# Kernel optimization log

Hardware: AMD Instinct MI355X
Metric: run time of the kernel (lower is better)

Reference implementation:

```python
import jax, jax.numpy as jnp
import numpy as np

NUM_CLASSES = 80
BBOX_W, OBJ_W, CLS_W = 2.0, 1.0, 0.5
ALPHA, GAMMA = 0.25, 2.0


def setup_inputs() -> dict:
    key = jax.random.key(0)
    ks = jax.random.split(key, 8)
    B, T = 32, 64
    return {
        "cls_p4": jax.random.normal(ks[0], (B, 1 + NUM_CLASSES, 80, 80), jnp.float32),
        "reg_p4": jax.random.normal(ks[1], (B, 4, 80, 80), jnp.float32),
        "cls_p5": jax.random.normal(ks[2], (B, 1 + NUM_CLASSES, 40, 40), jnp.float32),
        "reg_p5": jax.random.normal(ks[3], (B, 4, 40, 40), jnp.float32),
        "t4_cls": jax.random.randint(ks[4], (B, T), 0, NUM_CLASSES, jnp.int32),
        "t4_box": jax.random.uniform(ks[5], (B, T, 4), jnp.float32),
        "t4_mask": jnp.ones((B, T), jnp.float32),
        "t5_cls": jax.random.randint(ks[6], (B, T), 0, NUM_CLASSES, jnp.int32),
        "t5_box": jax.random.uniform(ks[7], (B, T, 4), jnp.float32),
        "t5_mask": jnp.ones((B, T), jnp.float32),
    }


def _bce_logits(x, t):
    # stable BCEWithLogits: log(1+e^x) - x*t
    return jnp.logaddexp(0.0, x) - x * t


def _scale_loss(cls_p, reg_p, cls_ids, box, mask):
    B, C, H, W = cls_p.shape
    tx = box[..., 0] * W  # [B,T]
    ty = box[..., 1] * H
    tw = box[..., 2] * W
    th = box[..., 3] * H
    gx = jnp.clip(tx, 0, W - 1).astype(jnp.int32)
    gy = jnp.clip(ty, 0, H - 1).astype(jnp.int32)
    bb = jnp.arange(B)[:, None]  # [B,1] broadcast over T

    # gather per-target reg/cls vectors: [B,T,4] and [B,T,C]
    rv = jnp.transpose(reg_p, (0, 2, 3, 1))[bb, gy, gx]
    cv = jnp.transpose(cls_p, (0, 2, 3, 1))[bb, gy, gx]

    dx = jax.nn.sigmoid(rv[..., 0])
    dy = jax.nn.sigmoid(rv[..., 1])
    dw = jnp.exp(jnp.clip(rv[..., 2], -4.0, 4.0))
    dh = jnp.exp(jnp.clip(rv[..., 3], -4.0, 4.0))
    px = gx.astype(jnp.float32) + dx
    py = gy.astype(jnp.float32) + dy
    pred_box = jnp.stack([px - dw / 2, py - dh / 2, px + dw / 2, py + dh / 2], -1)
    tgt_box = jnp.stack([tx - tw / 2, ty - th / 2, tx + tw / 2, ty + th / 2], -1)

    d = pred_box - tgt_box
    sl1 = jnp.where(jnp.abs(d) < 1.0, 0.5 * d * d, jnp.abs(d) - 0.5).mean(-1)  # [B,T]
    lb = (sl1 * mask).sum()

    # objectness loss at target cells (target = 1)
    obj_t = cv[..., 0]
    lo = (jax.nn.softplus(-obj_t) * mask).sum()

    # focal classification loss
    onehot = jax.nn.one_hot(cls_ids, C - 1, dtype=cls_p.dtype)  # [B,T,NC]
    logits = cv[..., 1:]
    bce = _bce_logits(logits, onehot)
    p = jax.nn.sigmoid(logits)
    pt = p * onehot + (1.0 - p) * (1.0 - onehot)
    focal = (ALPHA * (1.0 - pt) ** GAMMA * bce).mean(-1)  # [B,T]
    lc = (focal * mask).sum()

    n = mask.sum()

    # background objectness: cells not hit by any valid target
    obj_map = jnp.zeros((B, H, W), cls_p.dtype).at[bb, gy, gx].max(mask)
    bg = obj_map == 0
    bg_cnt = bg.sum()
    bce_bg = jnp.where(bg, jax.nn.softplus(cls_p[:, 0]), 0.0).sum()
    lo = lo + 0.05 * jnp.where(bg_cnt > 0, bce_bg / jnp.maximum(bg_cnt, 1), 0.0)
    return lb, lo, lc, n


def reference(cls_p4, reg_p4, cls_p5, reg_p5,
              t4_cls, t4_box, t4_mask, t5_cls, t5_box, t5_mask):
    lb4, lo4, lc4, n4 = _scale_loss(cls_p4, reg_p4, t4_cls, t4_box, t4_mask)
    lb5, lo5, lc5, n5 = _scale_loss(cls_p5, reg_p5, t5_cls, t5_box, t5_mask)
    lb, lo, lc, n = lb4 + lb5, lo4 + lo5, lc4 + lc5, n4 + n5
    lb = jnp.where(n > 0, lb / jnp.maximum(n, 1), lb)
    lc = jnp.where(n > 0, lc / jnp.maximum(n, 1), lc)
    lo = lo / jnp.maximum(n, 1.0)
    total = BBOX_W * lb + OBJ_W * lo + CLS_W * lc
    return total
```

## Files before the change

### kernel.cpp

```cpp
#include <hip/hip_runtime.h>
#include <math.h>

#define NUM_CLASSES 80
#define C_CH (NUM_CLASSES + 1)

__device__ __forceinline__ float softplusf(float x) {
    return fmaxf(x, 0.f) + log1pf(expf(-fabsf(x)));
}
__device__ __forceinline__ float sigmoidf_(float x) {
    return 1.f / (1.f + expf(-x));
}


__global__ void fused_kernel(
    const float* __restrict__ cls_p4, const float* __restrict__ reg_p4,
    const float* __restrict__ cls_p5, const float* __restrict__ reg_p5,
    const int* __restrict__ t4_cls, const float* __restrict__ t4_box, const float* __restrict__ t4_mask,
    const int* __restrict__ t5_cls, const float* __restrict__ t5_box, const float* __restrict__ t5_mask,
    float* __restrict__ bgpart, float* __restrict__ tpart,
    int B, int T, int nbg4, int nbg5)
{
    const int tid = threadIdx.x;
    const int nbg = nbg4 + nbg5;

    if ((int)blockIdx.x < nbg) {
        const int blk = blockIdx.x;
        float sp = 0.f;
        if (blk < nbg4) {
            int b = blk / 25, j = blk - b * 25;
            int cell = j * 256 + tid;
            sp = softplusf(cls_p4[(size_t)b * (C_CH * 6400) + cell]);
        } else {
            int o = blk - nbg4;
            int b = o / 7, j = o - b * 7;
            int cell = j * 256 + tid;
            if (cell < 1600)
                sp = softplusf(cls_p5[(size_t)b * (C_CH * 1600) + cell]);
        }
        for (int off = 32; off > 0; off >>= 1) sp += __shfl_down(sp, off, 64);
        __shared__ float ss[4];
        if ((tid & 63) == 0) ss[tid >> 6] = sp;
        __syncthreads();
        if (tid == 0) bgpart[blockIdx.x] = ss[0] + ss[1] + ss[2] + ss[3];
        return;
    }

    const int BT = B * T;
    const int wave = tid >> 6;
    const int lane = tid & 63;
    const int tg = ((int)blockIdx.x - nbg) * 4 + wave;

    float lb = 0.f, lo = 0.f, lcv = 0.f, msum = 0.f;

    if (tg < 2 * BT) {
        const int scale = (tg >= BT) ? 1 : 0;
        const int ti = scale ? tg - BT : tg;
        const int b = ti / T;

        const float* cls_p; const float* reg_p; const int* tc; const float* tb_; const float* tm;
        int H, W;
        if (!scale) { cls_p = cls_p4; reg_p = reg_p4; tc = t4_cls; tb_ = t4_box; tm = t4_mask; H = 80; W = 80; }
        else        { cls_p = cls_p5; reg_p = reg_p5; tc = t5_cls; tb_ = t5_box; tm = t5_mask; H = 40; W = 40; }
        const int HW = H * W;

        const float mask = tm[ti];
        const int   cid  = tc[ti];
        const float bx0 = tb_[ti * 4 + 0], bx1 = tb_[ti * 4 + 1];
        const float bx2 = tb_[ti * 4 + 2], bx3 = tb_[ti * 4 + 3];

        const float tx = bx0 * (float)W, ty = bx1 * (float)H;
        const float tw = bx2 * (float)W, th = bx3 * (float)H;
        const int gx = (int)fminf(fmaxf(tx, 0.f), (float)(W - 1));
        const int gy = (int)fminf(fmaxf(ty, 0.f), (float)(H - 1));
        const int cell = gy * W + gx;

        const float* cvbase = cls_p + (size_t)b * C_CH * HW + cell;

        float rvq = 0.f;
        if (lane < 4) rvq = reg_p[(size_t)(b * 4 + lane) * HW + cell];
        float objq = (lane == 0) ? cvbase[0] : 0.f;

        float fsum = 0.f;
        for (int c = lane; c < NUM_CLASSES; c += 64) {
            float x   = cvbase[(size_t)(c + 1) * HW];
            float tgt = (c == cid) ? 1.f : 0.f;
            float bce = softplusf(x) - x * tgt;
            float p   = sigmoidf_(x);
            float pt  = p * tgt + (1.f - p) * (1.f - tgt);
            float om  = 1.f - pt;
            fsum += 0.25f * om * om * bce;
        }
        for (int off = 32; off > 0; off >>= 1) fsum += __shfl_down(fsum, off, 64);

        float rv0 = __shfl(rvq, 0, 64), rv1 = __shfl(rvq, 1, 64);
        float rv2 = __shfl(rvq, 2, 64), rv3 = __shfl(rvq, 3, 64);

        if (lane == 0) {
            lcv = (fsum * (1.f / (float)NUM_CLASSES)) * mask;
            lo  = softplusf(-objq) * mask;

            float dx = sigmoidf_(rv0), dy = sigmoidf_(rv1);
            float dw = expf(fminf(fmaxf(rv2, -4.f), 4.f));
            float dh = expf(fminf(fmaxf(rv3, -4.f), 4.f));
            float px = (float)gx + dx, py = (float)gy + dy;
            float pb0 = px - dw * 0.5f, pb1 = py - dh * 0.5f, pb2 = px + dw * 0.5f, pb3 = py + dh * 0.5f;
            float tb0 = tx - tw * 0.5f, tb1 = ty - th * 0.5f, tb2 = tx + tw * 0.5f, tb3 = ty + th * 0.5f;
            float s = 0.f, d, a;
            d = pb0 - tb0; a = fabsf(d); s += (a < 1.f) ? 0.5f * d * d : a - 0.5f;
            d = pb1 - tb1; a = fabsf(d); s += (a < 1.f) ? 0.5f * d * d : a - 0.5f;
            d = pb2 - tb2; a = fabsf(d); s += (a < 1.f) ? 0.5f * d * d : a - 0.5f;
            d = pb3 - tb3; a = fabsf(d); s += (a < 1.f) ? 0.5f * d * d : a - 0.5f;
            lb = (s * 0.25f) * mask;
            msum = mask;
        }
    }

    __shared__ float s4[4][4];
    if (lane == 0) { s4[wave][0] = lb; s4[wave][1] = lo; s4[wave][2] = lcv; s4[wave][3] = msum; }
    __syncthreads();
    if (tid < 4) {
        float v = s4[0][tid] + s4[1][tid] + s4[2][tid] + s4[3][tid];
        tpart[((int)blockIdx.x - nbg) * 4 + tid] = v;
    }
}

#define HASH_SZ 8192

__global__ void __launch_bounds__(1024) final_kernel(
    const float* __restrict__ cls_p4, const float* __restrict__ cls_p5,
    const float* __restrict__ t4_box, const float* __restrict__ t4_mask,
    const float* __restrict__ t5_box, const float* __restrict__ t5_mask,
    const float* __restrict__ bgpart, int nbg4, int nbg5,
    const float* __restrict__ tpart, int nT4,
    int B, int T, float* __restrict__ out)
{
    __shared__ unsigned int hash[HASH_SZ];
    __shared__ float red[16][12];
    const int tid = threadIdx.x;
    const int BT = B * T;

    for (int i = tid; i < HASH_SZ; i += 1024) hash[i] = 0u;
    __syncthreads();

    float occ_sp4 = 0.f, occ_c4 = 0.f, occ_sp5 = 0.f, occ_c5 = 0.f;
    for (int g = tid; g < 2 * BT; g += 1024) {
        const int scale = (g >= BT) ? 1 : 0;
        const int ti = scale ? g - BT : g;
        const float* tb_ = scale ? t5_box : t4_box;
        const float* tm  = scale ? t5_mask : t4_mask;
        const float mask = tm[ti];
        if (mask > 0.f) {
            const int b = ti / T;
            const int W = scale ? 40 : 80, H = W;
            const int HW = W * H;
            const float tx = tb_[ti * 4 + 0] * (float)W;
            const float ty = tb_[ti * 4 + 1] * (float)H;
            const int gx = (int)fminf(fmaxf(tx, 0.f), (float)(W - 1));
            const int gy = (int)fminf(fmaxf(ty, 0.f), (float)(H - 1));
            const int cell = gy * W + gx;
            const unsigned int id = ((unsigned)scale << 18) | (unsigned)(b * HW + cell);
            const unsigned int key = id + 1u;
            unsigned int h = (id * 2654435761u) >> 19;
            h &= (HASH_SZ - 1);
            for (;;) {
                unsigned int old = atomicCAS(&hash[h], 0u, key);
                if (old == 0u) {
                    const float* cls_p = scale ? cls_p5 : cls_p4;
                    float sp = softplusf(cls_p[(size_t)b * C_CH * HW + cell]);
                    if (scale) { occ_sp5 += sp; occ_c5 += 1.f; }
                    else       { occ_sp4 += sp; occ_c4 += 1.f; }
                    break;
                }
                if (old == key) break;
                h = (h + 1) & (HASH_SZ - 1);
            }
        }
    }

    float lb = 0.f, lo = 0.f, lc = 0.f, n = 0.f, bg4 = 0.f, bg5 = 0.f;
    for (int i = tid; i < nT4; i += 1024) {
        lb += tpart[i * 4 + 0]; lo += tpart[i * 4 + 1];
        lc += tpart[i * 4 + 2]; n  += tpart[i * 4 + 3];
    }
    for (int i = tid; i < nbg4; i += 1024) bg4 += bgpart[i];
    for (int i = tid; i < nbg5; i += 1024) bg5 += bgpart[nbg4 + i];

    float vals[10] = { lb, lo, lc, n, bg4, bg5, occ_sp4, occ_c4, occ_sp5, occ_c5 };
    #pragma unroll
    for (int k = 0; k < 10; k++) {
        float v = vals[k];
        for (int off = 32; off > 0; off >>= 1) v += __shfl_down(v, off, 64);
        vals[k] = v;
    }
    if ((tid & 63) == 0) {
        #pragma unroll
        for (int k = 0; k < 10; k++) red[tid >> 6][k] = vals[k];
    }
    __syncthreads();
    if (tid == 0) {
        float t[10];
        #pragma unroll
        for (int k = 0; k < 10; k++) {
            float s = 0.f;
            for (int w = 0; w < 16; w++) s += red[w][k];
            t[k] = s;
        }
        float lbt = t[0], lot = t[1], lct = t[2], nt = t[3];
        float bce_bg4 = t[4] - t[6];
        float bce_bg5 = t[5] - t[8];
        float cnt4 = (float)(B * 6400) - t[7];
        float cnt5 = (float)(B * 1600) - t[9];
        lot += 0.05f * ((cnt4 > 0.f) ? bce_bg4 / fmaxf(cnt4, 1.f) : 0.f);
        lot += 0.05f * ((cnt5 > 0.f) ? bce_bg5 / fmaxf(cnt5, 1.f) : 0.f);
        float nd = fmaxf(nt, 1.f);
        if (nt > 0.f) { lbt /= nd; lct /= nd; }
        lot /= fmaxf(nt, 1.f);
        out[0] = 2.0f * lbt + 1.0f * lot + 0.5f * lct;
    }
}

extern "C" void kernel_launch(void* const* d_in, const int* in_sizes, int n_in,
                              void* d_out, int out_size, void* d_ws, size_t ws_size,
                              hipStream_t stream) {
    const float* cls_p4 = (const float*)d_in[0];
    const float* reg_p4 = (const float*)d_in[1];
    const float* cls_p5 = (const float*)d_in[2];
    const float* reg_p5 = (const float*)d_in[3];
    const int*   t4_cls = (const int*)d_in[4];
    const float* t4_box = (const float*)d_in[5];
    const float* t4_mask= (const float*)d_in[6];
    const int*   t5_cls = (const int*)d_in[7];
    const float* t5_box = (const float*)d_in[8];
    const float* t5_mask= (const float*)d_in[9];

    const int B = in_sizes[0] / (C_CH * 6400);
    const int T = in_sizes[4] / B;
    const int BT = B * T;

    const int nbg4 = B * 25;
    const int nbg5 = B * 7;
    const int nTblk = (2 * BT + 3) / 4;

    float* bgpart = (float*)d_ws;
    float* tpart  = bgpart + (nbg4 + nbg5);

    fused_kernel<<<nbg4 + nbg5 + nTblk, 256, 0, stream>>>(
        cls_p4, reg_p4, cls_p5, reg_p5,
        t4_cls, t4_box, t4_mask, t5_cls, t5_box, t5_mask,
        bgpart, tpart, B, T, nbg4, nbg5);

    final_kernel<<<1, 1024, 0, stream>>>(
        cls_p4, cls_p5, t4_box, t4_mask, t5_box, t5_mask,
        bgpart, nbg4, nbg5, tpart, nTblk, B, T, (float*)d_out);
}
```

Baseline: 148.0 us.

## Move occupied-cell dedup from single-block hash into parallel per-batch waves

Background-cell deduplication moves out of the single-block final kernel's shared-memory atomic hash table. Extra blocks in the main kernel now handle it, one wave per (scale, batch) pair, using a quadratic first-occurrence scan over the targets. The final kernel shrinks to a 256-thread reduction of partial sums. Targets per batch are capped at MAX_T; above that cap the occupied-cell correction is silently skipped.

```diff
diff --git a/kernel.cpp b/kernel.cpp
--- a/kernel.cpp
+++ b/kernel.cpp
@@ -3,6 +3,7 @@
 
 #define NUM_CLASSES 80
 #define C_CH (NUM_CLASSES + 1)
+#define MAX_T 128
 
 __device__ __forceinline__ float softplusf(float x) {
     return fmaxf(x, 0.f) + log1pf(expf(-fabsf(x)));
@@ -17,11 +18,14 @@
     const float* __restrict__ cls_p5, const float* __restrict__ reg_p5,
     const int* __restrict__ t4_cls, const float* __restrict__ t4_box, const float* __restrict__ t4_mask,
     const int* __restrict__ t5_cls, const float* __restrict__ t5_box, const float* __restrict__ t5_mask,
-    float* __restrict__ bgpart, float* __restrict__ tpart,
-    int B, int T, int nbg4, int nbg5)
+    float* __restrict__ bgpart, float* __restrict__ tpart, float* __restrict__ occpart,
+    int B, int T, int nbg4, int nbg5, int nTblk)
 {
-    const int tid = threadIdx.x;
-    const int nbg = nbg4 + nbg5;
+    const int tid  = threadIdx.x;
+    const int wave = tid >> 6;
+    const int lane = tid & 63;
+    const int nbg  = nbg4 + nbg5;
+    const int BT   = B * T;
 
     if ((int)blockIdx.x < nbg) {
         const int blk = blockIdx.x;
@@ -39,153 +43,165 @@
         }
         for (int off = 32; off > 0; off >>= 1) sp += __shfl_down(sp, off, 64);
         __shared__ float ss[4];
-        if ((tid & 63) == 0) ss[tid >> 6] = sp;
+        if (lane == 0) ss[wave] = sp;
         __syncthreads();
         if (tid == 0) bgpart[blockIdx.x] = ss[0] + ss[1] + ss[2] + ss[3];
         return;
     }
 
-    const int BT = B * T;
-    const int wave = tid >> 6;
-    const int lane = tid & 63;
-    const int tg = ((int)blockIdx.x - nbg) * 4 + wave;
-
-    float lb = 0.f, lo = 0.f, lcv = 0.f, msum = 0.f;
-
-    if (tg < 2 * BT) {
-        const int scale = (tg >= BT) ? 1 : 0;
-        const int ti = scale ? tg - BT : tg;
-        const int b = ti / T;
-
-        const float* cls_p; const float* reg_p; const int* tc; const float* tb_; const float* tm;
-        int H, W;
-        if (!scale) { cls_p = cls_p4; reg_p = reg_p4; tc = t4_cls; tb_ = t4_box; tm = t4_mask; H = 80; W = 80; }
-        else        { cls_p = cls_p5; reg_p = reg_p5; tc = t5_cls; tb_ = t5_box; tm = t5_mask; H = 40; W = 40; }
-        const int HW = H * W;
-
-        const float mask = tm[ti];
-        const int   cid  = tc[ti];
-        const float bx0 = tb_[ti * 4 + 0], bx1 = tb_[ti * 4 + 1];
-        const float bx2 = tb_[ti * 4 + 2], bx3 = tb_[ti * 4 + 3];
-
-        const float tx = bx0 * (float)W, ty = bx1 * (float)H;
-        const float tw = bx2 * (float)W, th = bx3 * (float)H;
-        const int gx = (int)fminf(fmaxf(tx, 0.f), (float)(W - 1));
-        const int gy = (int)fminf(fmaxf(ty, 0.f), (float)(H - 1));
-        const int cell = gy * W + gx;
-
-        const float* cvbase = cls_p + (size_t)b * C_CH * HW + cell;
-
-        float rvq = 0.f;
-        if (lane < 4) rvq = reg_p[(size_t)(b * 4 + lane) * HW + cell];
-        float objq = (lane == 0) ? cvbase[0] : 0.f;
-
-        float fsum = 0.f;
-        for (int c = lane; c < NUM_CLASSES; c += 64) {
-            float x   = cvbase[(size_t)(c + 1) * HW];
-            float tgt = (c == cid) ? 1.f : 0.f;
-            float bce = softplusf(x) - x * tgt;
-            float p   = sigmoidf_(x);
-            float pt  = p * tgt + (1.f - p) * (1.f - tgt);
-            float om  = 1.f - pt;
-            fsum += 0.25f * om * om * bce;
-        }
-        for (int off = 32; off > 0; off >>= 1) fsum += __shfl_down(fsum, off, 64);
-
-        float rv0 = __shfl(rvq, 0, 64), rv1 = __shfl(rvq, 1, 64);
-        float rv2 = __shfl(rvq, 2, 64), rv3 = __shfl(rvq, 3, 64);
-
-        if (lane == 0) {
-            lcv = (fsum * (1.f / (float)NUM_CLASSES)) * mask;
-            lo  = softplusf(-objq) * mask;
-
-            float dx = sigmoidf_(rv0), dy = sigmoidf_(rv1);
-            float dw = expf(fminf(fmaxf(rv2, -4.f), 4.f));
-            float dh = expf(fminf(fmaxf(rv3, -4.f), 4.f));
-            float px = (float)gx + dx, py = (float)gy + dy;
-            float pb0 = px - dw * 0.5f, pb1 = py - dh * 0.5f, pb2 = px + dw * 0.5f, pb3 = py + dh * 0.5f;
-            float tb0 = tx - tw * 0.5f, tb1 = ty - th * 0.5f, tb2 = tx + tw * 0.5f, tb3 = ty + th * 0.5f;
-            float s = 0.f, d, a;
-            d = pb0 - tb0; a = fabsf(d); s += (a < 1.f) ? 0.5f * d * d : a - 0.5f;
-            d = pb1 - tb1; a = fabsf(d); s += (a < 1.f) ? 0.5f * d * d : a - 0.5f;
-            d = pb2 - tb2; a = fabsf(d); s += (a < 1.f) ? 0.5f * d * d : a - 0.5f;
-            d = pb3 - tb3; a = fabsf(d); s += (a < 1.f) ? 0.5f * d * d : a - 0.5f;
-            lb = (s * 0.25f) * mask;
-            msum = mask;
-        }
-    }
-
-    __shared__ float s4[4][4];
-    if (lane == 0) { s4[wave][0] = lb; s4[wave][1] = lo; s4[wave][2] = lcv; s4[wave][3] = msum; }
-    __syncthreads();
-    if (tid < 4) {
-        float v = s4[0][tid] + s4[1][tid] + s4[2][tid] + s4[3][tid];
-        tpart[((int)blockIdx.x - nbg) * 4 + tid] = v;
-    }
-}
-
-#define HASH_SZ 8192
-
-__global__ void __launch_bounds__(1024) final_kernel(
-    const float* __restrict__ cls_p4, const float* __restrict__ cls_p5,
-    const float* __restrict__ t4_box, const float* __restrict__ t4_mask,
-    const float* __restrict__ t5_box, const float* __restrict__ t5_mask,
-    const float* __restrict__ bgpart, int nbg4, int nbg5,
-    const float* __restrict__ tpart, int nT4,
-    int B, int T, float* __restrict__ out)
-{
-    __shared__ unsigned int hash[HASH_SZ];
-    __shared__ float red[16][12];
-    const int tid = threadIdx.x;
-    const int BT = B * T;
-
-    for (int i = tid; i < HASH_SZ; i += 1024) hash[i] = 0u;
-    __syncthreads();
-
-    float occ_sp4 = 0.f, occ_c4 = 0.f, occ_sp5 = 0.f, occ_c5 = 0.f;
-    for (int g = tid; g < 2 * BT; g += 1024) {
-        const int scale = (g >= BT) ? 1 : 0;
-        const int ti = scale ? g - BT : g;
-        const float* tb_ = scale ? t5_box : t4_box;
-        const float* tm  = scale ? t5_mask : t4_mask;
-        const float mask = tm[ti];
-        if (mask > 0.f) {
+    if ((int)blockIdx.x < nbg + nTblk) {
+        const int tg = ((int)blockIdx.x - nbg) * 4 + wave;
+        float lb = 0.f, lo = 0.f, lcv = 0.f, msum = 0.f;
+
+        if (tg < 2 * BT) {
+            const int scale = (tg >= BT) ? 1 : 0;
+            const int ti = scale ? tg - BT : tg;
             const int b = ti / T;
-            const int W = scale ? 40 : 80, H = W;
-            const int HW = W * H;
-            const float tx = tb_[ti * 4 + 0] * (float)W;
-            const float ty = tb_[ti * 4 + 1] * (float)H;
+
+            const float* cls_p; const float* reg_p; const int* tc; const float* tb_; const float* tm;
+            int H, W;
+            if (!scale) { cls_p = cls_p4; reg_p = reg_p4; tc = t4_cls; tb_ = t4_box; tm = t4_mask; H = 80; W = 80; }
+            else        { cls_p = cls_p5; reg_p = reg_p5; tc = t5_cls; tb_ = t5_box; tm = t5_mask; H = 40; W = 40; }
+            const int HW = H * W;
+
+            const float mask = tm[ti];
+            const int   cid  = tc[ti];
+            const float bx0 = tb_[ti * 4 + 0], bx1 = tb_[ti * 4 + 1];
+            const float bx2 = tb_[ti * 4 + 2], bx3 = tb_[ti * 4 + 3];
+
+            const float tx = bx0 * (float)W, ty = bx1 * (float)H;
+            const float tw = bx2 * (float)W, th = bx3 * (float)H;
             const int gx = (int)fminf(fmaxf(tx, 0.f), (float)(W - 1));
             const int gy = (int)fminf(fmaxf(ty, 0.f), (float)(H - 1));
             const int cell = gy * W + gx;
-            const unsigned int id = ((unsigned)scale << 18) | (unsigned)(b * HW + cell);
-            const unsigned int key = id + 1u;
-            unsigned int h = (id * 2654435761u) >> 19;
-            h &= (HASH_SZ - 1);
-            for (;;) {
-                unsigned int old = atomicCAS(&hash[h], 0u, key);
-                if (old == 0u) {
-                    const float* cls_p = scale ? cls_p5 : cls_p4;
-                    float sp = softplusf(cls_p[(size_t)b * C_CH * HW + cell]);
-                    if (scale) { occ_sp5 += sp; occ_c5 += 1.f; }
-                    else       { occ_sp4 += sp; occ_c4 += 1.f; }
-                    break;
+
+            const float* cvbase = cls_p + (size_t)b * C_CH * HW + cell;
+
+            float rvq = 0.f;
+            if (lane < 4) rvq = reg_p[(size_t)(b * 4 + lane) * HW + cell];
+            float objq = (lane == 0) ? cvbase[0] : 0.f;
+
+            float fsum = 0.f;
+            for (int c = lane; c < NUM_CLASSES; c += 64) {
+                float x   = cvbase[(size_t)(c + 1) * HW];
+                float tgt = (c == cid) ? 1.f : 0.f;
+                float bce = softplusf(x) - x * tgt;
+                float p   = sigmoidf_(x);
+                float pt  = p * tgt + (1.f - p) * (1.f - tgt);
+                float om  = 1.f - pt;
+                fsum += 0.25f * om * om * bce;
+            }
+            for (int off = 32; off > 0; off >>= 1) fsum += __shfl_down(fsum, off, 64);
+
+            float rv0 = __shfl(rvq, 0, 64), rv1 = __shfl(rvq, 1, 64);
+            float rv2 = __shfl(rvq, 2, 64), rv3 = __shfl(rvq, 3, 64);
+
+            if (lane == 0) {
+                lcv = (fsum * (1.f / (float)NUM_CLASSES)) * mask;
+                lo  = softplusf(-objq) * mask;
+
+                float dx = sigmoidf_(rv0), dy = sigmoidf_(rv1);
+                float dw = expf(fminf(fmaxf(rv2, -4.f), 4.f));
+                float dh = expf(fminf(fmaxf(rv3, -4.f), 4.f));
+                float px = (float)gx + dx, py = (float)gy + dy;
+                float pb0 = px - dw * 0.5f, pb1 = py - dh * 0.5f, pb2 = px + dw * 0.5f, pb3 = py + dh * 0.5f;
+                float tb0 = tx - tw * 0.5f, tb1 = ty - th * 0.5f, tb2 = tx + tw * 0.5f, tb3 = ty + th * 0.5f;
+                float s = 0.f, d, a;
+                d = pb0 - tb0; a = fabsf(d); s += (a < 1.f) ? 0.5f * d * d : a - 0.5f;
+                d = pb1 - tb1; a = fabsf(d); s += (a < 1.f) ? 0.5f * d * d : a - 0.5f;
+                d = pb2 - tb2; a = fabsf(d); s += (a < 1.f) ? 0.5f * d * d : a - 0.5f;
+                d = pb3 - tb3; a = fabsf(d); s += (a < 1.f) ? 0.5f * d * d : a - 0.5f;
+                lb = (s * 0.25f) * mask;
+                msum = mask;
+            }
+        }
+
+        __shared__ float s4[4][4];
+        if (lane == 0) { s4[wave][0] = lb; s4[wave][1] = lo; s4[wave][2] = lcv; s4[wave][3] = msum; }
+        __syncthreads();
+        if (tid < 4) {
+            float v = s4[0][tid] + s4[1][tid] + s4[2][tid] + s4[3][tid];
+            tpart[((int)blockIdx.x - nbg) * 4 + tid] = v;
+        }
+        return;
+    }
+
+    {
+        __shared__ unsigned int cells[4][MAX_T];
+        const int p = ((int)blockIdx.x - nbg - nTblk) * 4 + wave;
+        float osp = 0.f, ocnt = 0.f;
+        bool valid_pair = (p < 2 * B) && (T <= MAX_T);
+        int scale = 0, b = 0;
+        const float* tb_ = nullptr; const float* tm = nullptr;
+        int W = 80, HW = 6400;
+        if (valid_pair) {
+            scale = p / B; b = p - scale * B;
+            tb_ = scale ? t5_box : t4_box;
+            tm  = scale ? t5_mask : t4_mask;
+            W = scale ? 40 : 80; HW = W * W;
+            for (int i = lane; i < T; i += 64) {
+                const int ti = b * T + i;
+                unsigned int cellv = 0xFFFFFFFFu;
+                if (tm[ti] > 0.f) {
+                    const float tx = tb_[ti * 4 + 0] * (float)W;
+                    const float ty = tb_[ti * 4 + 1] * (float)W;
+                    const int gx = (int)fminf(fmaxf(tx, 0.f), (float)(W - 1));
+                    const int gy = (int)fminf(fmaxf(ty, 0.f), (float)(W - 1));
+                    cellv = (unsigned)(gy * W + gx);
                 }
-                if (old == key) break;
-                h = (h + 1) & (HASH_SZ - 1);
-            }
-        }
-    }
-
-    float lb = 0.f, lo = 0.f, lc = 0.f, n = 0.f, bg4 = 0.f, bg5 = 0.f;
-    for (int i = tid; i < nT4; i += 1024) {
+                cells[wave][i] = cellv;
+            }
+        }
+        __syncthreads();
+        if (valid_pair) {
+            const float* cls_p = scale ? cls_p5 : cls_p4;
+            for (int i = lane; i < T; i += 64) {
+                unsigned int cv = cells[wave][i];
+                if (cv != 0xFFFFFFFFu) {
+                    bool first = true;
+                    for (int j = 0; j < i; j++)
+                        if (cells[wave][j] == cv) { first = false; break; }
+                    if (first) {
+                        osp  += softplusf(cls_p[(size_t)b * C_CH * HW + (int)cv]);
+                        ocnt += 1.f;
+                    }
+                }
+            }
+        }
+        for (int off = 32; off > 0; off >>= 1) {
+            osp  += __shfl_down(osp,  off, 64);
+            ocnt += __shfl_down(ocnt, off, 64);
+        }
+        if (lane == 0 && p < 2 * B) {
+            occpart[p * 2]     = osp;
+            occpart[p * 2 + 1] = ocnt;
+        }
+    }
+}
+
+__global__ void __launch_bounds__(256) final_kernel(
+    const float* __restrict__ bgpart, int nbg4, int nbg5,
+    const float* __restrict__ tpart, int nTblk,
+    const float* __restrict__ occpart,
+    int B, float* __restrict__ out)
+{
+    const int tid = threadIdx.x;
+    float lb = 0.f, lo = 0.f, lc = 0.f, n = 0.f;
+    float bg4 = 0.f, bg5 = 0.f, o4 = 0.f, c4 = 0.f, o5 = 0.f, c5 = 0.f;
+
+    for (int i = tid; i < nTblk; i += 256) {
         lb += tpart[i * 4 + 0]; lo += tpart[i * 4 + 1];
         lc += tpart[i * 4 + 2]; n  += tpart[i * 4 + 3];
     }
-    for (int i = tid; i < nbg4; i += 1024) bg4 += bgpart[i];
-    for (int i = tid; i < nbg5; i += 1024) bg5 += bgpart[nbg4 + i];
-
-    float vals[10] = { lb, lo, lc, n, bg4, bg5, occ_sp4, occ_c4, occ_sp5, occ_c5 };
+    for (int i = tid; i < nbg4; i += 256) bg4 += bgpart[i];
+    for (int i = tid; i < nbg5; i += 256) bg5 += bgpart[nbg4 + i];
+    for (int p = tid; p < 2 * B; p += 256) {
+        if (p < B) { o4 += occpart[p * 2]; c4 += occpart[p * 2 + 1]; }
+        else       { o5 += occpart[p * 2]; c5 += occpart[p * 2 + 1]; }
+    }
+
+    __shared__ float red[4][10];
+    float vals[10] = { lb, lo, lc, n, bg4, bg5, o4, c4, o5, c5 };
     #pragma unroll
     for (int k = 0; k < 10; k++) {
         float v = vals[k];
@@ -200,11 +216,9 @@
     if (tid == 0) {
         float t[10];
         #pragma unroll
-        for (int k = 0; k < 10; k++) {
-            float s = 0.f;
-            for (int w = 0; w < 16; w++) s += red[w][k];
-            t[k] = s;
-        }
+        for (int k = 0; k < 10; k++)
+            t[k] = red[0][k] + red[1][k] + red[2][k] + red[3][k];
+
         float lbt = t[0], lot = t[1], lct = t[2], nt = t[3];
         float bce_bg4 = t[4] - t[6];
         float bce_bg5 = t[5] - t[8];
@@ -237,19 +251,20 @@
     const int T = in_sizes[4] / B;
     const int BT = B * T;
 
-    const int nbg4 = B * 25;
-    const int nbg5 = B * 7;
+    const int nbg4  = B * 25;
+    const int nbg5  = B * 7;
     const int nTblk = (2 * BT + 3) / 4;
-
-    float* bgpart = (float*)d_ws;
-    float* tpart  = bgpart + (nbg4 + nbg5);
-
-    fused_kernel<<<nbg4 + nbg5 + nTblk, 256, 0, stream>>>(
+    const int ndblk = (2 * B + 3) / 4;
+
+    float* bgpart  = (float*)d_ws;
+    float* tpart   = bgpart + (nbg4 + nbg5);
+    float* occpart = tpart + (size_t)nTblk * 4;
+
+    fused_kernel<<<nbg4 + nbg5 + nTblk + ndblk, 256, 0, stream>>>(
         cls_p4, reg_p4, cls_p5, reg_p5,
         t4_cls, t4_box, t4_mask, t5_cls, t5_box, t5_mask,
-        bgpart, tpart, B, T, nbg4, nbg5);
-
-    final_kernel<<<1, 1024, 0, stream>>>(
-        cls_p4, cls_p5, t4_box, t4_mask, t5_box, t5_mask,
-        bgpart, nbg4, nbg5, tpart, nTblk, B, T, (float*)d_out);
-}
+        bgpart, tpart, occpart, B, T, nbg4, nbg5, nTblk);
+
+    final_kernel<<<1, 256, 0, stream>>>(bgpart, nbg4, nbg5, tpart, nTblk,
+                                        occpart, B, (float*)d_out);
+}
```

New measurement: 126.8 us (median of 2 runs). -14.3%, faster.
